# Kernel optimization log

Measured on AMD Instinct MI355X. Metric: run time of the kernel, lower is better.

Reference implementation:

```python
import jax, jax.numpy as jnp
import numpy as np

EPS = 1e-10
FAR_DELTA = 1e10  # delta appended for the last sample, as in the torch code


def setup_inputs() -> dict:
    key = jax.random.key(0)
    k1, k2, k3 = jax.random.split(key, 3)
    N, P, C = 131072, 128, 3
    density = jax.random.normal(k1, (N, P), dtype=jnp.float32)  # raw density (relu'd inside)
    feature = jax.random.uniform(k2, (N, P, C), dtype=jnp.float32)
    # depth values must be increasing along the sample dim (they come from a ray sampler);
    # build them as a cumulative sum of positive steps in roughly [0, 6].
    steps = jax.random.uniform(k3, (N, P), dtype=jnp.float32) * 0.05
    depth_values = jnp.cumsum(steps, axis=-1) + 1.0
    return {"density": density, "feature": feature, "depth_values": depth_values}


def reference(density, feature, depth_values):
    # deltas: consecutive depth differences, huge delta for the final sample  [N, P]
    deltas = jnp.concatenate(
        [depth_values[:, 1:] - depth_values[:, :-1],
         jnp.full_like(depth_values[:, :1], FAR_DELTA)], axis=-1)
    # alpha = 1 - exp(-relu(density) * delta)   [N, P]
    alpha = 1.0 - jnp.exp(-jax.nn.relu(density) * deltas)
    # transmittance: exclusive cumprod of (1 - alpha + eps)   [N, P]
    trans = jnp.cumprod(
        jnp.concatenate([jnp.ones_like(alpha[:, :1]), 1.0 - alpha + EPS], axis=-1),
        axis=-1)[:, :-1]
    weights = alpha * trans  # [N, P]
    feat_out = jnp.sum(weights[..., None] * feature, axis=1)  # [N, C]
    depth_out = jnp.sum(weights * depth_values, axis=1)       # [N]
    return feat_out, depth_out
```

## Files before the change

### kernel.cpp

```cpp
#include <hip/hip_runtime.h>

#define EPS 1e-10f
#define FAR_DELTA 1e10f

__global__ __launch_bounds__(256, 8) void volrend_kernel(
    const float* __restrict__ density,
    const float* __restrict__ feature,
    const float* __restrict__ depth,
    float* __restrict__ feat_out,
    float* __restrict__ depth_out,
    int N)
{
    __shared__ __align__(16) float featLDS[4 * 1536];

    const int tid  = threadIdx.x;
    const int lane = tid & 63;
    const int wv   = tid >> 6;
    const int j    = lane & 15;
    const int sub  = lane >> 4;
    const int r0   = blockIdx.x * 16 + wv * 4;
    const int ray  = r0 + sub;
    if (ray >= N) return;

    const float4* d4 = (const float4*)(density + (size_t)ray * 128 + j * 8);
    const float4* z4 = (const float4*)(depth   + (size_t)ray * 128 + j * 8);
    float4 dA = d4[0], dB = d4[1];
    float4 zA = z4[0], zB = z4[1];

    {
        const char* gb = (const char*)(feature + (size_t)r0 * 384) + lane * 16;
        char*       lb = (char*)&featLDS[wv * 1536];
        #pragma unroll
        for (int i = 0; i < 6; ++i) {
            __builtin_amdgcn_global_load_lds(
                (const __attribute__((address_space(1))) void*)(gb + i * 1024),
                (__attribute__((address_space(3))) void*)(lb + i * 1024),
                16, 0, 0);
        }
    }

    float z[8]  = {zA.x, zA.y, zA.z, zA.w, zB.x, zB.y, zB.z, zB.w};
    float dn[8] = {dA.x, dA.y, dA.z, dA.w, dB.x, dB.y, dB.z, dB.w};

    float znext = __shfl_down(z[0], 1, 64);

    float wl[8];
    float tl  = 1.0f;
    float adP = 0.0f;
    #pragma unroll
    for (int k = 0; k < 8; ++k) {
        float delta = (k < 7) ? (z[k + 1] - z[k])
                              : ((j == 15) ? FAR_DELTA : (znext - z[7]));
        float ex = __expf(-fmaxf(dn[k], 0.0f) * delta);
        float tk = ex + EPS;
        wl[k] = (1.0f - ex) * tl;
        adP  += wl[k] * z[k];
        tl   *= tk;
    }

    float s = tl;
    #pragma unroll
    for (int off = 1; off < 16; off <<= 1) {
        float v = __shfl_up(s, off, 16);
        if (j >= off) s *= v;
    }
    float excl = __shfl_up(s, 1, 16);
    if (j == 0) excl = 1.0f;

    __syncthreads();

    const float4* fl = (const float4*)&featLDS[wv * 1536 + sub * 384 + j * 24];
    float4 F0 = fl[0], F1 = fl[1], F2 = fl[2], F3 = fl[3], F4 = fl[4], F5 = fl[5];
    float f[24] = {F0.x, F0.y, F0.z, F0.w, F1.x, F1.y, F1.z, F1.w,
                   F2.x, F2.y, F2.z, F2.w, F3.x, F3.y, F3.z, F3.w,
                   F4.x, F4.y, F4.z, F4.w, F5.x, F5.y, F5.z, F5.w};

    float a0 = 0.0f, a1 = 0.0f, a2 = 0.0f;
    #pragma unroll
    for (int k = 0; k < 8; ++k) {
        a0 += wl[k] * f[3 * k + 0];
        a1 += wl[k] * f[3 * k + 1];
        a2 += wl[k] * f[3 * k + 2];
    }

    a0 *= excl; a1 *= excl; a2 *= excl;
    float ad = adP * excl;

    #pragma unroll
    for (int off = 8; off >= 1; off >>= 1) {
        a0 += __shfl_xor(a0, off, 16);
        a1 += __shfl_xor(a1, off, 16);
        a2 += __shfl_xor(a2, off, 16);
        ad += __shfl_xor(ad, off, 16);
    }

    if (j == 0) {
        feat_out[(size_t)ray * 3 + 0] = a0;
        feat_out[(size_t)ray * 3 + 1] = a1;
        feat_out[(size_t)ray * 3 + 2] = a2;
        depth_out[ray] = ad;
    }
}

extern "C" void kernel_launch(void* const* d_in, const int* in_sizes, int n_in,
                              void* d_out, int out_size, void* d_ws, size_t ws_size,
                              hipStream_t stream) {
    const float* density = (const float*)d_in[0];
    const float* feature = (const float*)d_in[1];
    const float* depth   = (const float*)d_in[2];

    const int P = 128;
    const int N = in_sizes[0] / P;

    float* feat_out  = (float*)d_out;
    float* depth_out = (float*)d_out + (size_t)N * 3;

    dim3 grid((N + 15) / 16);
    dim3 block(256);
    volrend_kernel<<<grid, block, 0, stream>>>(density, feature, depth,
                                               feat_out, depth_out, N);
}
```

Measured before the change: 353.7 us.

## Use persistent grid-stride blocks with register double-buffered prefetch of next tile

Replaces the one-tile-per-block launch with a fixed grid of 1024 persistent blocks that loop over 16-ray tiles. Inside the loop, the density, depth and feature data for the next tile are prefetched into registers while the current tile is computed. Feature data is now read straight from global memory into registers instead of going through LDS via global_load_lds, which removes the __syncthreads. The cost is higher register pressure (launch bounds lowered to 4) and uncoalesced 96-byte-strided feature loads per lane. The tail guard is also dropped, so it assumes N is a multiple of 16.

```diff
diff --git a/kernel.cpp b/kernel.cpp
--- a/kernel.cpp
+++ b/kernel.cpp
@@ -3,102 +3,114 @@
 #define EPS 1e-10f
 #define FAR_DELTA 1e10f
 
-__global__ __launch_bounds__(256, 8) void volrend_kernel(
+__global__ __launch_bounds__(256, 4) void volrend_kernel(
     const float* __restrict__ density,
     const float* __restrict__ feature,
     const float* __restrict__ depth,
     float* __restrict__ feat_out,
     float* __restrict__ depth_out,
-    int N)
+    int N, int numW)
 {
-    __shared__ __align__(16) float featLDS[4 * 1536];
-
     const int tid  = threadIdx.x;
     const int lane = tid & 63;
     const int wv   = tid >> 6;
     const int j    = lane & 15;
     const int sub  = lane >> 4;
-    const int r0   = blockIdx.x * 16 + wv * 4;
-    const int ray  = r0 + sub;
-    if (ray >= N) return;
+    const int roff = wv * 4 + sub;
 
-    const float4* d4 = (const float4*)(density + (size_t)ray * 128 + j * 8);
-    const float4* z4 = (const float4*)(depth   + (size_t)ray * 128 + j * 8);
-    float4 dA = d4[0], dB = d4[1];
-    float4 zA = z4[0], zB = z4[1];
+    int w = blockIdx.x;
+    if (w >= numW) return;
+
+    float4 cdA, cdB, czA, czB, cF0, cF1, cF2, cF3, cF4, cF5;
+    float4 ndA, ndB, nzA, nzB, nF0, nF1, nF2, nF3, nF4, nF5;
 
     {
-        const char* gb = (const char*)(feature + (size_t)r0 * 384) + lane * 16;
-        char*       lb = (char*)&featLDS[wv * 1536];
-        #pragma unroll
-        for (int i = 0; i < 6; ++i) {
-            __builtin_amdgcn_global_load_lds(
-                (const __attribute__((address_space(1))) void*)(gb + i * 1024),
-                (__attribute__((address_space(3))) void*)(lb + i * 1024),
-                16, 0, 0);
-        }
+        const int ray = w * 16 + roff;
+        const float4* d4 = (const float4*)(density + (size_t)ray * 128 + j * 8);
+        const float4* z4 = (const float4*)(depth   + (size_t)ray * 128 + j * 8);
+        const float4* f4 = (const float4*)(feature + (size_t)ray * 384 + j * 24);
+        cdA = d4[0]; cdB = d4[1]; czA = z4[0]; czB = z4[1];
+        cF0 = f4[0]; cF1 = f4[1]; cF2 = f4[2]; cF3 = f4[3]; cF4 = f4[4]; cF5 = f4[5];
     }
 
-    float z[8]  = {zA.x, zA.y, zA.z, zA.w, zB.x, zB.y, zB.z, zB.w};
-    float dn[8] = {dA.x, dA.y, dA.z, dA.w, dB.x, dB.y, dB.z, dB.w};
+    while (w < numW) {
+        const int wn = w + gridDim.x;
 
-    float znext = __shfl_down(z[0], 1, 64);
+        {
+            const int wp  = (wn < numW) ? wn : w;
+            const int ray = wp * 16 + roff;
+            const float4* d4 = (const float4*)(density + (size_t)ray * 128 + j * 8);
+            const float4* z4 = (const float4*)(depth   + (size_t)ray * 128 + j * 8);
+            const float4* f4 = (const float4*)(feature + (size_t)ray * 384 + j * 24);
+            ndA = d4[0]; ndB = d4[1]; nzA = z4[0]; nzB = z4[1];
+            nF0 = f4[0]; nF1 = f4[1]; nF2 = f4[2]; nF3 = f4[3]; nF4 = f4[4]; nF5 = f4[5];
+        }
 
-    float wl[8];
-    float tl  = 1.0f;
-    float adP = 0.0f;
-    #pragma unroll
-    for (int k = 0; k < 8; ++k) {
-        float delta = (k < 7) ? (z[k + 1] - z[k])
-                              : ((j == 15) ? FAR_DELTA : (znext - z[7]));
-        float ex = __expf(-fmaxf(dn[k], 0.0f) * delta);
-        float tk = ex + EPS;
-        wl[k] = (1.0f - ex) * tl;
-        adP  += wl[k] * z[k];
-        tl   *= tk;
-    }
+        {
+            const int ray = w * 16 + roff;
 
-    float s = tl;
-    #pragma unroll
-    for (int off = 1; off < 16; off <<= 1) {
-        float v = __shfl_up(s, off, 16);
-        if (j >= off) s *= v;
-    }
-    float excl = __shfl_up(s, 1, 16);
-    if (j == 0) excl = 1.0f;
+            float z[8]  = {czA.x, czA.y, czA.z, czA.w, czB.x, czB.y, czB.z, czB.w};
+            float dn[8] = {cdA.x, cdA.y, cdA.z, cdA.w, cdB.x, cdB.y, cdB.z, cdB.w};
 
-    __syncthreads();
+            float znext = __shfl_down(z[0], 1, 64);
 
-    const float4* fl = (const float4*)&featLDS[wv * 1536 + sub * 384 + j * 24];
-    float4 F0 = fl[0], F1 = fl[1], F2 = fl[2], F3 = fl[3], F4 = fl[4], F5 = fl[5];
-    float f[24] = {F0.x, F0.y, F0.z, F0.w, F1.x, F1.y, F1.z, F1.w,
-                   F2.x, F2.y, F2.z, F2.w, F3.x, F3.y, F3.z, F3.w,
-                   F4.x, F4.y, F4.z, F4.w, F5.x, F5.y, F5.z, F5.w};
+            float wl[8];
+            float tl  = 1.0f;
+            float adP = 0.0f;
+            #pragma unroll
+            for (int k = 0; k < 8; ++k) {
+                float delta = (k < 7) ? (z[k + 1] - z[k])
+                                      : ((j == 15) ? FAR_DELTA : (znext - z[7]));
+                float ex = __expf(-fmaxf(dn[k], 0.0f) * delta);
+                float tk = ex + EPS;
+                wl[k] = (1.0f - ex) * tl;
+                adP  += wl[k] * z[k];
+                tl   *= tk;
+            }
 
-    float a0 = 0.0f, a1 = 0.0f, a2 = 0.0f;
-    #pragma unroll
-    for (int k = 0; k < 8; ++k) {
-        a0 += wl[k] * f[3 * k + 0];
-        a1 += wl[k] * f[3 * k + 1];
-        a2 += wl[k] * f[3 * k + 2];
-    }
+            float s = tl;
+            #pragma unroll
+            for (int off = 1; off < 16; off <<= 1) {
+                float v = __shfl_up(s, off, 16);
+                if (j >= off) s *= v;
+            }
+            float excl = __shfl_up(s, 1, 16);
+            if (j == 0) excl = 1.0f;
 
-    a0 *= excl; a1 *= excl; a2 *= excl;
-    float ad = adP * excl;
+            float f[24] = {cF0.x, cF0.y, cF0.z, cF0.w, cF1.x, cF1.y, cF1.z, cF1.w,
+                           cF2.x, cF2.y, cF2.z, cF2.w, cF3.x, cF3.y, cF3.z, cF3.w,
+                           cF4.x, cF4.y, cF4.z, cF4.w, cF5.x, cF5.y, cF5.z, cF5.w};
 
-    #pragma unroll
-    for (int off = 8; off >= 1; off >>= 1) {
-        a0 += __shfl_xor(a0, off, 16);
-        a1 += __shfl_xor(a1, off, 16);
-        a2 += __shfl_xor(a2, off, 16);
-        ad += __shfl_xor(ad, off, 16);
-    }
+            float a0 = 0.0f, a1 = 0.0f, a2 = 0.0f;
+            #pragma unroll
+            for (int k = 0; k < 8; ++k) {
+                a0 += wl[k] * f[3 * k + 0];
+                a1 += wl[k] * f[3 * k + 1];
+                a2 += wl[k] * f[3 * k + 2];
+            }
 
-    if (j == 0) {
-        feat_out[(size_t)ray * 3 + 0] = a0;
-        feat_out[(size_t)ray * 3 + 1] = a1;
-        feat_out[(size_t)ray * 3 + 2] = a2;
-        depth_out[ray] = ad;
+            a0 *= excl; a1 *= excl; a2 *= excl;
+            float ad = adP * excl;
+
+            #pragma unroll
+            for (int off = 8; off >= 1; off >>= 1) {
+                a0 += __shfl_xor(a0, off, 16);
+                a1 += __shfl_xor(a1, off, 16);
+                a2 += __shfl_xor(a2, off, 16);
+                ad += __shfl_xor(ad, off, 16);
+            }
+
+            if (j == 0) {
+                feat_out[(size_t)ray * 3 + 0] = a0;
+                feat_out[(size_t)ray * 3 + 1] = a1;
+                feat_out[(size_t)ray * 3 + 2] = a2;
+                depth_out[ray] = ad;
+            }
+        }
+
+        cdA = ndA; cdB = ndB; czA = nzA; czB = nzB;
+        cF0 = nF0; cF1 = nF1; cF2 = nF2; cF3 = nF3; cF4 = nF4; cF5 = nF5;
+        w = wn;
     }
 }
 
@@ -115,8 +127,9 @@
     float* feat_out  = (float*)d_out;
     float* depth_out = (float*)d_out + (size_t)N * 3;
 
-    dim3 grid((N + 15) / 16);
-    dim3 block(256);
-    volrend_kernel<<<grid, block, 0, stream>>>(density, feature, depth,
-                                               feat_out, depth_out, N);
+    const int numW = (N + 15) / 16;
+    int grid = 1024;
+    if (grid > numW) grid = numW;
+    volrend_kernel<<<dim3(grid), dim3(256), 0, stream>>>(
+        density, feature, depth, feat_out, depth_out, N, numW);
 }
```

Result: no change. 355.5 us (+0.5%).
